# Performance work log

Hardware: AMD Instinct MI355X
Metric: run time of the kernel (lower is better)

The kernel has to match this reference:

```python
import jax, jax.numpy as jnp
import numpy as np

EPS = 1e-5
NUM_HEADS = 8
POOL_K = 50
POOL_S = 15
DEPTH = 4


def _conv2d(x, w, b, pad_h, pad_w):
    y = jax.lax.conv_general_dilated(
        x, w, window_strides=(1, 1),
        padding=((pad_h, pad_h), (pad_w, pad_w)),
        dimension_numbers=('NCHW', 'OIHW', 'NCHW'))
    return y + b[None, :, None, None]


def _bn_eval(x, g, b):
    # eval-mode BatchNorm2d with running_mean=0, running_var=1
    s = g / jnp.sqrt(1.0 + EPS)
    return x * s[None, :, None, None] + b[None, :, None, None]


def _layernorm(x, g, b):
    m = x.mean(-1, keepdims=True)
    v = ((x - m) ** 2).mean(-1, keepdims=True)
    return (x - m) / jnp.sqrt(v + EPS) * g + b


def _mha(x, wq, bq, wk, bk, wv, bv, wo, bo):
    B, n, d = x.shape
    def split(h):
        return h.reshape(B, n, NUM_HEADS, -1).transpose(0, 2, 1, 3)  # b h n dk
    q = split(x @ wq.T + bq)
    k = split(x @ wk.T + bk)
    v = split(x @ wv.T + bv)
    dk = q.shape[-1]
    scores = jnp.einsum('bhqd,bhkd->bhqk', q, k) / jnp.sqrt(jnp.float32(dk))
    attn = jax.nn.softmax(scores, axis=-1)
    o = jnp.einsum('bhqk,bhkd->bhqd', attn, v).transpose(0, 2, 1, 3).reshape(B, n, d)
    return o @ wo.T + bo


def _encoder(x, p):
    (g1, b1, g2, b2, wq, bq, wk, bk, wv, bv, wo, bo, f1w, f1b, f2w, f2b) = p
    h = _layernorm(x, g1, b1)
    x = x + _mha(h, wq, bq, wk, bk, wv, bv, wo, bo)
    h = _layernorm(x, g2, b2)
    ff = jax.nn.gelu(h @ f1w.T + f1b, approximate=False) @ f2w.T + f2b
    return x + ff


def _forward(x, tw1, tb1, tw2, tb2, tw3, tb3, tw4, tb4, bn1_g, bn1_b, sw, sb,
             bn2_g, bn2_b, ln1_g, ln1_b, ln2_g, ln2_b, wq, bq, wk, bk, wv, bv,
             wo, bo, f1w, f1b, f2w, f2b, ew, eb, bn3_g, bn3_b, cw, cb):
    B, C, T = x.shape
    xi = x[:, None]  # [B,1,C,T]
    h = jnp.concatenate([
        _conv2d(xi, tw1, tb1, 0, 7),
        _conv2d(xi, tw2, tb2, 0, 12),
        _conv2d(xi, tw3, tb3, 0, 25),
        _conv2d(xi, tw4, tb4, 0, 32)], axis=1)          # [B,D,C,T]
    h = _bn_eval(h, bn1_g, bn1_b)
    h = _conv2d(h, sw, sb, 0, 0)                         # [B,D,1,T]
    h = jax.nn.elu(_bn_eval(h, bn2_g, bn2_b))[:, :, 0]   # [B,D,T]

    npos = (T - POOL_K) // POOL_S + 1
    idx = np.arange(npos)[:, None] * POOL_S + np.arange(POOL_K)  # [n,K]
    win = h[:, :, idx]                                   # [B,D,n,K]
    avg = win.mean(-1)                                   # [B,D,n]
    var = win.var(-1, ddof=1)                            # unbiased, like torch
    vlog = jnp.log(jnp.clip(var, 1e-6, 1e6))
    x1 = avg.transpose(0, 2, 1)                          # [B,n,D]
    x2 = vlog.transpose(0, 2, 1)

    for i in range(DEPTH):
        p = (ln1_g[i], ln1_b[i], ln2_g[i], ln2_b[i], wq[i], bq[i], wk[i], bk[i],
             wv[i], bv[i], wo[i], bo[i], f1w[i], f1b[i], f2w[i], f2b[i])
        x1 = _encoder(x1, p)
        x2 = _encoder(x2, p)

    h = jnp.concatenate([x1[:, :, None, :], x2[:, :, None, :]], axis=2)  # [B,n,2,D]
    h = jax.nn.elu(_bn_eval(_conv2d(h, ew, eb, 0, 0), bn3_g, bn3_b))     # [B,n,1,D]
    return h.reshape(B, -1) @ cw.T + cb


def setup_inputs() -> dict:
    B, C, T, D, n, ff, ncls = 16, 64, 1000, 128, 64, 512, 4
    ks = iter(jax.random.split(jax.random.key(0), 48))
    def nrm(shape, s=0.02):
        return jax.random.normal(next(ks), shape, jnp.float32) * s
    inp = {
        'x': jax.random.normal(next(ks), (B, C, T), jnp.float32),
        'tw1': nrm((D // 4, 1, 1, 15)), 'tb1': jnp.zeros(D // 4),
        'tw2': nrm((D // 4, 1, 1, 25)), 'tb2': jnp.zeros(D // 4),
        'tw3': nrm((D // 4, 1, 1, 51)), 'tb3': jnp.zeros(D // 4),
        'tw4': nrm((D // 4, 1, 1, 65)), 'tb4': jnp.zeros(D // 4),
        'bn1_g': jnp.ones(D), 'bn1_b': jnp.zeros(D),
        'sw': nrm((D, D, C, 1)), 'sb': jnp.zeros(D),
        'bn2_g': jnp.ones(D), 'bn2_b': jnp.zeros(D),
        'ln1_g': jnp.ones((DEPTH, D)), 'ln1_b': jnp.zeros((DEPTH, D)),
        'ln2_g': jnp.ones((DEPTH, D)), 'ln2_b': jnp.zeros((DEPTH, D)),
        'wq': nrm((DEPTH, D, D)), 'bq': jnp.zeros((DEPTH, D)),
        'wk': nrm((DEPTH, D, D)), 'bk': jnp.zeros((DEPTH, D)),
        'wv': nrm((DEPTH, D, D)), 'bv': jnp.zeros((DEPTH, D)),
        'wo': nrm((DEPTH, D, D)), 'bo': jnp.zeros((DEPTH, D)),
        'f1w': nrm((DEPTH, ff, D)), 'f1b': jnp.zeros((DEPTH, ff)),
        'f2w': nrm((DEPTH, D, ff)), 'f2b': jnp.zeros((DEPTH, D)),
        'ew': nrm((n, n, 2, 1)), 'eb': jnp.zeros(n),
        'bn3_g': jnp.ones(n), 'bn3_b': jnp.zeros(n),
        'cw': nrm((ncls, D * n)), 'cb': jnp.zeros(ncls),
    }
    return inp


def reference(x, tw1, tb1, tw2, tb2, tw3, tb3, tw4, tb4, bn1_g, bn1_b, sw, sb,
              bn2_g, bn2_b, ln1_g, ln1_b, ln2_g, ln2_b, wq, bq, wk, bk, wv, bv,
              wo, bo, f1w, f1b, f2w, f2b, ew, eb, bn3_g, bn3_b, cw, cb):
    return _forward(x, tw1, tb1, tw2, tb2, tw3, tb3, tw4, tb4, bn1_g, bn1_b,
                    sw, sb, bn2_g, bn2_b, ln1_g, ln1_b, ln2_g, ln2_b, wq, bq,
                    wk, bk, wv, bv, wo, bo, f1w, f1b, f2w, f2b, ew, eb,
                    bn3_g, bn3_b, cw, cb)
```

## Files before the change

### kernel.cpp

```cpp
#include <hip/hip_runtime.h>
#include <math.h>

typedef unsigned short u16;
typedef __attribute__((ext_vector_type(8))) short frag8;
typedef __attribute__((ext_vector_type(4))) float f32x4;

__device__ __forceinline__ float eluf(float v) { return v > 0.f ? v : expm1f(v); }
__device__ __forceinline__ float geluf(float v) {
  return 0.5f * v * (1.f + erff(v * 0.70710678118654752f));
}
__device__ __forceinline__ u16 f2bf(float f) {
  union { float f; unsigned int i; } v; v.f = f;
  return (u16)((v.i + 0x7fffu + ((v.i >> 16) & 1u)) >> 16);
}

#define BN_S 0.99999500003749969f

__global__ void k_tws1(const float* tw1, const float* tw2, const float* tw3, const float* tw4,
                       const float* tb1, const float* tb2, const float* tb3, const float* tb4,
                       const float* bn1g, const float* bn1b,
                       float* tws1, float* c1) {
  int idx = blockIdx.x * 256 + threadIdx.x;
  if (idx < 8320) {
    int i = idx / 65, u = idx - i * 65;
    int g = i >> 5, il = i & 31;
    const float* tws[4] = {tw1, tw2, tw3, tw4};
    const int P[4] = {7, 12, 25, 32};
    int c = u - 32;
    float s1 = bn1g[i] * BN_S;
    float val = 0.f;
    int p = P[g];
    if (c >= -p && c <= p) val = s1 * tws[g][il * (2 * p + 1) + (c + p)];
    tws1[idx] = val;
  } else if (idx < 8448) {
    int i = idx - 8320;
    int g = i >> 5, il = i & 31;
    const float* tbs[4] = {tb1, tb2, tb3, tb4};
    float s1 = bn1g[i] * BN_S;
    c1[i] = s1 * tbs[g][il] + bn1b[i];
  }
}

__global__ __launch_bounds__(256) void k_weff(const float* __restrict__ sw, const float* __restrict__ sb,
                                              const float* __restrict__ tws1, const float* __restrict__ c1,
                                              u16* __restrict__ Wb, float* __restrict__ biasEff) {
  __shared__ float swl[8192];
  __shared__ float tl[8320];
  const int tid = threadIdx.x, lane = tid & 63, wave = tid >> 6;
  const int o = blockIdx.x;
  for (int idx = tid; idx < 8192; idx += 256) swl[idx] = sw[o * 8192 + idx];
  for (int idx = tid; idx < 8320; idx += 256) tl[idx] = tws1[idx];
  __syncthreads();

  #pragma unroll 1
  for (int j = 0; j < 4; j++) {
    int u0 = (wave + 4 * j) * 4;
    float a[4][4];
    #pragma unroll
    for (int uu = 0; uu < 4; uu++)
      #pragma unroll
      for (int r = 0; r < 4; r++) a[uu][r] = 0.f;
    #pragma unroll 1
    for (int i = 0; i < 128; i += 4) {
      #pragma unroll
      for (int ii = 0; ii < 4; ii++) {
        float s = swl[(i + ii) * 64 + lane];
        #pragma unroll
        for (int uu = 0; uu < 4; uu++)
          a[uu][ii] = fmaf(s, tl[(i + ii) * 65 + u0 + uu], a[uu][ii]);
      }
    }
    #pragma unroll
    for (int uu = 0; uu < 4; uu++)
      Wb[((u0 + uu) * 128 + o) * 64 + lane] = f2bf((a[uu][0] + a[uu][1]) + (a[uu][2] + a[uu][3]));
  }

  if (wave == 0) {
    float a[4] = {0.f, 0.f, 0.f, 0.f};
    #pragma unroll 1
    for (int i = 0; i < 128; i += 4) {
      #pragma unroll
      for (int ii = 0; ii < 4; ii++)
        a[ii] = fmaf(swl[(i + ii) * 64 + lane], tl[(i + ii) * 65 + 64], a[ii]);
    }
    Wb[(64 * 128 + o) * 64 + lane] = f2bf((a[0] + a[1]) + (a[2] + a[3]));
  } else if (wave == 1) {
    float pa = 0.f;
    #pragma unroll 8
    for (int i = 0; i < 128; i++)
      pa = fmaf(swl[i * 64 + lane], c1[i], pa);
    #pragma unroll
    for (int off = 32; off; off >>= 1) pa += __shfl_xor(pa, off);
    if (lane == 0) biasEff[o] = pa + sb[o];
  }
}

__global__ __launch_bounds__(256) void k_conv(const float* __restrict__ x,
                                              const u16* __restrict__ Wb,
                                              const float* __restrict__ biasEff,
                                              const float* __restrict__ bn2g, const float* __restrict__ bn2b,
                                              float* __restrict__ z) {
  __shared__ u16 xs[128 * 88];
  const int tid = threadIdx.x;
  const int t0 = blockIdx.x * 64;
  const int o0 = blockIdx.y * 32;
  const int b  = blockIdx.z;

  #pragma unroll
  for (int i = 0; i < 8; i++) {
    int pos = tid + i * 256;
    int kh = pos >> 5;
    int tt = (pos & 31) * 4;
    int gt = t0 - 32 + tt;
    const float* xp = x + (b * 64 + kh) * 1000;
    float v[4];
    if (gt >= 0 && gt + 3 < 1000) {
      float4 f = *(const float4*)(xp + gt);
      v[0] = f.x; v[1] = f.y; v[2] = f.z; v[3] = f.w;
    } else {
      #pragma unroll
      for (int e = 0; e < 4; e++) { int g2 = gt + e; v[e] = (g2 >= 0 && g2 < 1000) ? xp[g2] : 0.f; }
    }
    #pragma unroll
    for (int e = 0; e < 4; e++) xs[(tt + e) * 88 + kh] = f2bf(v[e]);
  }
  __syncthreads();

  const int lane = tid & 63, wave = tid >> 6;
  const int wt = (wave & 1) * 32;
  const int wo = (wave >> 1) * 16;
  const int m = lane & 15, q = lane >> 4;

  f32x4 acc[2];
  #pragma unroll
  for (int i = 0; i < 2; i++) acc[i] = (f32x4){0.f, 0.f, 0.f, 0.f};

  #pragma unroll 2
  for (int u = 0; u < 65; u++) {
    frag8 A[2][2], B[2];
    #pragma unroll
    for (int tp = 0; tp < 2; tp++)
      #pragma unroll
      for (int kc = 0; kc < 2; kc++)
        A[tp][kc] = *(const frag8*)&xs[(wt + tp * 16 + m + u) * 88 + kc * 32 + q * 8];
    #pragma unroll
    for (int kc = 0; kc < 2; kc++)
      B[kc] = *(const frag8*)(Wb + ((u * 128) + o0 + wo + m) * 64 + kc * 32 + q * 8);
    #pragma unroll
    for (int tp = 0; tp < 2; tp++) {
      acc[tp] = __builtin_amdgcn_mfma_f32_16x16x32_bf16(A[tp][0], B[0], acc[tp], 0, 0, 0);
      acc[tp] = __builtin_amdgcn_mfma_f32_16x16x32_bf16(A[tp][1], B[1], acc[tp], 0, 0, 0);
    }
  }

  {
    int o = o0 + wo + m;
    float s2 = bn2g[o] * BN_S;
    float be = biasEff[o], b2 = bn2b[o];
    #pragma unroll
    for (int tp = 0; tp < 2; tp++) {
      #pragma unroll
      for (int r = 0; r < 4; r++) {
        int t = t0 + wt + tp * 16 + q * 4 + r;
        if (t < 1000)
          z[(b * 128 + o) * 1000 + t] = eluf((acc[tp][r] + be) * s2 + b2);
      }
    }
  }
}

__global__ __launch_bounds__(256) void k_pool(const float* __restrict__ z, float* __restrict__ X) {
  __shared__ float zl[16 * 1001];
  int b = blockIdx.x, og = blockIdx.y;
  int tid = threadIdx.x;
  const float* zb = z + (b * 128 + og * 16) * 1000;
  #pragma unroll 1
  for (int r = 0; r < 16; r++)
    for (int c = tid; c < 1000; c += 256) zl[r * 1001 + c] = zb[r * 1000 + c];
  __syncthreads();

  int ol = tid & 15;
  int pb = tid >> 4;
  #pragma unroll 1
  for (int pass = 0; pass < 4; pass++) {
    int p = pb + pass * 16;
    const float* zp = zl + ol * 1001 + p * 15;
    float s = 0.f, ss = 0.f;
    #pragma unroll
    for (int k = 0; k < 50; k++) { float v = zp[k]; s += v; ss = fmaf(v, v, ss); }
    float m = s * 0.02f;
    float var = (ss - s * m) * (1.f / 49.f);
    var = fminf(fmaxf(var, 1e-6f), 1e6f);
    int o = og * 16 + ol;
    X[(b * 64 + p) * 128 + o] = m;
    X[((16 + b) * 64 + p) * 128 + o] = logf(var);
  }
}

__global__ __launch_bounds__(256) void k_cvt6(const float* __restrict__ wq, const float* __restrict__ wk,
                                              const float* __restrict__ wv, const float* __restrict__ wo,
                                              const float* __restrict__ f1w, const float* __restrict__ f2w,
                                              u16* __restrict__ out) {
  int i = blockIdx.x * 256 + threadIdx.x;
  if (i >= 196608) return;
  int fi = i * 4;
  const float* src; int off;
  if      (fi < 65536)  { src = wq;  off = fi; }
  else if (fi < 131072) { src = wk;  off = fi - 65536; }
  else if (fi < 196608) { src = wv;  off = fi - 131072; }
  else if (fi < 262144) { src = wo;  off = fi - 196608; }
  else if (fi < 524288) { src = f1w; off = fi - 262144; }
  else                  { src = f2w; off = fi - 524288; }
  float4 v = *(const float4*)(src + off);
  ushort4 p;
  p.x = f2bf(v.x); p.y = f2bf(v.y); p.z = f2bf(v.z); p.w = f2bf(v.w);
  *(ushort4*)(out + fi) = p;
}

__device__ __forceinline__ void ln128(const float* __restrict__ Xs, u16* __restrict__ Hs,
                                      const float* __restrict__ g, const float* __restrict__ b,
                                      int lane, int wave) {
  float g0 = g[lane], g1 = g[64 + lane], b0 = b[lane], b1 = b[64 + lane];
  #pragma unroll
  for (int rr = 0; rr < 8; rr++) {
    int r = wave * 8 + rr;
    float v0 = Xs[r * 132 + lane], v1 = Xs[r * 132 + 64 + lane];
    float s_ = v0 + v1;
    #pragma unroll
    for (int off = 32; off; off >>= 1) s_ += __shfl_xor(s_, off);
    float mn = s_ * (1.f / 128.f);
    float d0 = v0 - mn, d1 = v1 - mn;
    float qq = d0 * d0 + d1 * d1;
    #pragma unroll
    for (int off = 32; off; off >>= 1) qq += __shfl_xor(qq, off);
    float rs = rsqrtf(qq * (1.f / 128.f) + 1e-5f);
    Hs[r * 136 + lane]      = f2bf(d0 * rs * g0 + b0);
    Hs[r * 136 + 64 + lane] = f2bf(d1 * rs * g1 + b1);
  }
}

__device__ __forceinline__ void gemm_pref(const u16* __restrict__ Asrc, int astride,
                                          const frag8 Bf[4], int m, int q, f32x4 acc[4]) {
  #pragma unroll
  for (int kc = 0; kc < 4; kc++) {
    #pragma unroll
    for (int mt = 0; mt < 4; mt++) {
      frag8 Af = *(const frag8*)(Asrc + (mt * 16 + m) * astride + kc * 32 + q * 8);
      acc[mt] = __builtin_amdgcn_mfma_f32_16x16x32_bf16(Af, Bf[kc], acc[mt], 0, 0, 0);
    }
  }
}

__global__ __launch_bounds__(512, 1) void k_enc(float* __restrict__ X,
                                                const u16* __restrict__ Wenc,
                                                const float* __restrict__ ln1g, const float* __restrict__ ln1b,
                                                const float* __restrict__ ln2g, const float* __restrict__ ln2b,
                                                const float* __restrict__ bq, const float* __restrict__ bk,
                                                const float* __restrict__ bv, const float* __restrict__ bo,
                                                const float* __restrict__ f1b, const float* __restrict__ f2b) {
  __shared__ float Xs[64 * 132];
  __shared__ u16   Hs[64 * 136];
  __shared__ float QKV[3 * 64 * 132];
  float* Qs = QKV;
  float* Ks = QKV + 64 * 132;
  float* Vs = QKV + 2 * 64 * 132;
  u16* AOs  = Hs;
  u16* F1a  = (u16*)QKV;
  u16* F1b_ = (u16*)QKV + 64 * 136;

  const int tid = threadIdx.x;
  const int lane = tid & 63, wave = tid >> 6;
  const int m = lane & 15, q = lane >> 4;
  const int n0 = wave * 16;
  float* Xg = X + blockIdx.x * 64 * 128;

  const u16* WQ  = Wenc;
  const u16* WK  = Wenc + 65536;
  const u16* WV  = Wenc + 131072;
  const u16* WO  = Wenc + 196608;
  const u16* F1W = Wenc + 262144;
  const u16* F2W = Wenc + 524288;

  for (int i = tid; i < 8192; i += 512) Xs[(i >> 7) * 132 + (i & 127)] = Xg[i];
  __syncthreads();

  #pragma unroll 1
  for (int l = 0; l < 4; l++) {
    const u16* wqb  = WQ  + l * 16384;
    const u16* wkb  = WK  + l * 16384;
    const u16* wvb  = WV  + l * 16384;
    const u16* wob  = WO  + l * 16384;
    const u16* f1wb = F1W + l * 65536;
    const u16* f2wb = F2W + l * 65536;

    frag8 fq[4], fk[4], fv[4];
    #pragma unroll
    for (int kc = 0; kc < 4; kc++) {
      fq[kc] = *(const frag8*)(wqb + (n0 + m) * 128 + kc * 32 + q * 8);
      fk[kc] = *(const frag8*)(wkb + (n0 + m) * 128 + kc * 32 + q * 8);
      fv[kc] = *(const frag8*)(wvb + (n0 + m) * 128 + kc * 32 + q * 8);
    }

    ln128(Xs, Hs, ln1g + l * 128, ln1b + l * 128, lane, wave);
    __syncthreads();

    frag8 fo[4];
    #pragma unroll
    for (int kc = 0; kc < 4; kc++)
      fo[kc] = *(const frag8*)(wob + (n0 + m) * 128 + kc * 32 + q * 8);
    {
      f32x4 aq[4], ak[4], av[4];
      #pragma unroll
      for (int mt = 0; mt < 4; mt++) { aq[mt] = (f32x4){0,0,0,0}; ak[mt] = (f32x4){0,0,0,0}; av[mt] = (f32x4){0,0,0,0}; }
      gemm_pref(Hs, 136, fq, m, q, aq);
      gemm_pref(Hs, 136, fk, m, q, ak);
      gemm_pref(Hs, 136, fv, m, q, av);
      float bqv = bq[l * 128 + n0 + m];
      float bkv = bk[l * 128 + n0 + m];
      float bvv = bv[l * 128 + n0 + m];
      #pragma unroll
      for (int mt = 0; mt < 4; mt++)
        #pragma unroll
        for (int r = 0; r < 4; r++) {
          int row = mt * 16 + q * 4 + r;
          Qs[row * 132 + n0 + m] = aq[mt][r] + bqv;
          Ks[row * 132 + n0 + m] = ak[mt][r] + bkv;
          Vs[row * 132 + n0 + m] = av[mt][r] + bvv;
        }
    }
    __syncthreads();

    frag8 f1f[4];
    #pragma unroll
    for (int kc = 0; kc < 4; kc++)
      f1f[kc] = *(const frag8*)(f1wb + (n0 + m) * 128 + kc * 32 + q * 8);
    {
      const int h = wave, qr = lane;
      float qv[16];
      {
        const float4* qp = (const float4*)(Qs + qr * 132 + h * 16);
        #pragma unroll
        for (int j = 0; j < 4; j++) {
          float4 t = qp[j];
          qv[j * 4 + 0] = t.x; qv[j * 4 + 1] = t.y; qv[j * 4 + 2] = t.z; qv[j * 4 + 3] = t.w;
        }
      }
      const float* kbase = Ks + h * 16;
      const float* vbase = Vs + h * 16;
      float s_[64];
      float m0 = -1e30f, m1 = -1e30f, m2 = -1e30f, m3 = -1e30f;
      #pragma unroll
      for (int k4 = 0; k4 < 64; k4 += 4) {
        #pragma unroll
        for (int e = 0; e < 4; e++) {
          const float4* kp = (const float4*)(kbase + (k4 + e) * 132);
          float4 k0 = kp[0], k1 = kp[1], k2 = kp[2], k3 = kp[3];
          float d0 = qv[0] * k0.x + qv[1] * k0.y + qv[2] * k0.z + qv[3] * k0.w;
          float d1 = qv[4] * k1.x + qv[5] * k1.y + qv[6] * k1.z + qv[7] * k1.w;
          float d2 = qv[8] * k2.x + qv[9] * k2.y + qv[10] * k2.z + qv[11] * k2.w;
          float d3 = qv[12] * k3.x + qv[13] * k3.y + qv[14] * k3.z + qv[15] * k3.w;
          float sc = ((d0 + d1) + (d2 + d3)) * 0.25f;
          s_[k4 + e] = sc;
          if (e == 0) m0 = fmaxf(m0, sc);
          else if (e == 1) m1 = fmaxf(m1, sc);
          else if (e == 2) m2 = fmaxf(m2, sc);
          else m3 = fmaxf(m3, sc);
        }
      }
      float mx = fmaxf(fmaxf(m0, m1), fmaxf(m2, m3));
      float l_ = 0.f;
      float o[16];
      #pragma unroll
      for (int j = 0; j < 16; j++) o[j] = 0.f;
      #pragma unroll
      for (int k = 0; k < 64; k++) {
        float p = __expf(s_[k] - mx);
        l_ += p;
        const float4* vp = (const float4*)(vbase + k * 132);
        float4 v0 = vp[0], v1 = vp[1], v2 = vp[2], v3 = vp[3];
        o[0]  = fmaf(p, v0.x, o[0]);  o[1]  = fmaf(p, v0.y, o[1]);
        o[2]  = fmaf(p, v0.z, o[2]);  o[3]  = fmaf(p, v0.w, o[3]);
        o[4]  = fmaf(p, v1.x, o[4]);  o[5]  = fmaf(p, v1.y, o[5]);
        o[6]  = fmaf(p, v1.z, o[6]);  o[7]  = fmaf(p, v1.w, o[7]);
        o[8]  = fmaf(p, v2.x, o[8]);  o[9]  = fmaf(p, v2.y, o[9]);
        o[10] = fmaf(p, v2.z, o[10]); o[11] = fmaf(p, v2.w, o[11]);
        o[12] = fmaf(p, v3.x, o[12]); o[13] = fmaf(p, v3.y, o[13]);
        o[14] = fmaf(p, v3.z, o[14]); o[15] = fmaf(p, v3.w, o[15]);
      }
      float inv = 1.f / l_;
      u16* aop = AOs + qr * 136 + h * 16;
      #pragma unroll
      for (int j = 0; j < 16; j++) aop[j] = f2bf(o[j] * inv);
    }
    __syncthreads();

    {
      f32x4 ao4[4];
      #pragma unroll
      for (int mt = 0; mt < 4; mt++) ao4[mt] = (f32x4){0,0,0,0};
      gemm_pref(AOs, 136, fo, m, q, ao4);
      float bov = bo[l * 128 + n0 + m];
      #pragma unroll
      for (int mt = 0; mt < 4; mt++)
        #pragma unroll
        for (int r = 0; r < 4; r++)
          Xs[(mt * 16 + q * 4 + r) * 132 + n0 + m] += ao4[mt][r] + bov;
    }
    __syncthreads();

    ln128(Xs, Hs, ln2g + l * 128, ln2b + l * 128, lane, wave);
    __syncthreads();

    {
      f32x4 acc2[4];
      #pragma unroll
      for (int mt = 0; mt < 4; mt++) acc2[mt] = (f32x4){0,0,0,0};
      #pragma unroll 1
      for (int c = 0; c < 4; c++) {
        frag8 f2f[4];
        #pragma unroll
        for (int kc = 0; kc < 4; kc++)
          f2f[kc] = *(const frag8*)(f2wb + (n0 + m) * 512 + c * 128 + kc * 32 + q * 8);
        u16* F1c = (c & 1) ? F1b_ : F1a;
        {
          f32x4 a1[4];
          #pragma unroll
          for (int mt = 0; mt < 4; mt++) a1[mt] = (f32x4){0,0,0,0};
          gemm_pref(Hs, 136, f1f, m, q, a1);
          float b1v = f1b[l * 512 + c * 128 + n0 + m];
          #pragma unroll
          for (int mt = 0; mt < 4; mt++)
            #pragma unroll
            for (int r = 0; r < 4; r++)
              F1c[(mt * 16 + q * 4 + r) * 136 + n0 + m] = f2bf(geluf(a1[mt][r] + b1v));
        }
        __syncthreads();
        if (c < 3) {
          #pragma unroll
          for (int kc = 0; kc < 4; kc++)
            f1f[kc] = *(const frag8*)(f1wb + ((c + 1) * 128 + n0 + m) * 128 + kc * 32 + q * 8);
        }
        gemm_pref(F1c, 136, f2f, m, q, acc2);
      }
      float b2v = f2b[l * 128 + n0 + m];
      #pragma unroll
      for (int mt = 0; mt < 4; mt++)
        #pragma unroll
        for (int r = 0; r < 4; r++)
          Xs[(mt * 16 + q * 4 + r) * 132 + n0 + m] += acc2[mt][r] + b2v;
    }
    __syncthreads();
  }

  for (int i = tid; i < 8192; i += 512) Xg[i] = Xs[(i >> 7) * 132 + (i & 127)];
}

__global__ __launch_bounds__(256) void k_head1(const float* __restrict__ X, const float* __restrict__ ew,
                                               const float* __restrict__ eb, const float* __restrict__ g3,
                                               const float* __restrict__ b3, float* __restrict__ G) {
  __shared__ float Xs[2][8192];
  int b = blockIdx.x, ot = blockIdx.y;
  int tid = threadIdx.x;
  {
    const float4* x1 = (const float4*)(X + b * 8192);
    const float4* x2 = (const float4*)(X + (16 + b) * 8192);
    float4* s1 = (float4*)&Xs[0][0];
    float4* s2 = (float4*)&Xs[1][0];
    for (int i = tid; i < 2048; i += 256) { s1[i] = x1[i]; s2[i] = x2[i]; }
  }
  __syncthreads();
  int w = tid & 127, og = tid >> 7;
  int oc0 = ot * 16 + og * 8;
  float a[8] = {};
  for (int ic = 0; ic < 64; ic++) {
    float x1v = Xs[0][ic * 128 + w], x2v = Xs[1][ic * 128 + w];
    #pragma unroll
    for (int j = 0; j < 8; j++) {
      a[j] = fmaf(ew[((oc0 + j) * 64 + ic) * 2 + 0], x1v, a[j]);
      a[j] = fmaf(ew[((oc0 + j) * 64 + ic) * 2 + 1], x2v, a[j]);
    }
  }
  #pragma unroll
  for (int j = 0; j < 8; j++) {
    int oc = oc0 + j;
    float v = (a[j] + eb[oc]) * (g3[oc] * BN_S) + b3[oc];
    G[(b * 64 + oc) * 128 + w] = eluf(v);
  }
}

__global__ __launch_bounds__(256) void k_head2(const float* __restrict__ G, const float* __restrict__ cw,
                                               const float* __restrict__ cb, float* __restrict__ out) {
  __shared__ float red[256];
  int b = blockIdx.x, c = blockIdx.y, tid = threadIdx.x;
  const float4* g4 = (const float4*)(G + b * 8192);
  const float4* c4 = (const float4*)(cw + c * 8192);
  float p = 0.f;
  for (int i = tid; i < 2048; i += 256) {
    float4 g = g4[i], w = c4[i];
    p += g.x * w.x + g.y * w.y + g.z * w.z + g.w * w.w;
  }
  red[tid] = p;
  __syncthreads();
  for (int s = 128; s > 0; s >>= 1) {
    if (tid < s) red[tid] += red[tid + s];
    __syncthreads();
  }
  if (tid == 0) out[b * 4 + c] = red[0] + cb[c];
}

extern "C" void kernel_launch(void* const* d_in, const int* in_sizes, int n_in,
                              void* d_out, int out_size, void* d_ws, size_t ws_size,
                              hipStream_t stream) {
  const float* x    = (const float*)d_in[0];
  const float* tw1  = (const float*)d_in[1];  const float* tb1 = (const float*)d_in[2];
  const float* tw2  = (const float*)d_in[3];  const float* tb2 = (const float*)d_in[4];
  const float* tw3  = (const float*)d_in[5];  const float* tb3 = (const float*)d_in[6];
  const float* tw4  = (const float*)d_in[7];  const float* tb4 = (const float*)d_in[8];
  const float* bn1g = (const float*)d_in[9];  const float* bn1b = (const float*)d_in[10];
  const float* sw   = (const float*)d_in[11]; const float* sb   = (const float*)d_in[12];
  const float* bn2g = (const float*)d_in[13]; const float* bn2b = (const float*)d_in[14];
  const float* ln1g = (const float*)d_in[15]; const float* ln1b = (const float*)d_in[16];
  const float* ln2g = (const float*)d_in[17]; const float* ln2b = (const float*)d_in[18];
  const float* wq   = (const float*)d_in[19]; const float* bq   = (const float*)d_in[20];
  const float* wk   = (const float*)d_in[21]; const float* bk   = (const float*)d_in[22];
  const float* wv   = (const float*)d_in[23]; const float* bv   = (const float*)d_in[24];
  const float* wo   = (const float*)d_in[25]; const float* bo   = (const float*)d_in[26];
  const float* f1w  = (const float*)d_in[27]; const float* f1b  = (const float*)d_in[28];
  const float* f2w  = (const float*)d_in[29]; const float* f2b  = (const float*)d_in[30];
  const float* ew   = (const float*)d_in[31]; const float* eb   = (const float*)d_in[32];
  const float* g3   = (const float*)d_in[33]; const float* b3   = (const float*)d_in[34];
  const float* cw   = (const float*)d_in[35]; const float* cb   = (const float*)d_in[36];

  float* ws      = (float*)d_ws;
  float* tws1    = ws;
  float* c1      = ws + 8320;
  float* biasEff = ws + 8448;
  u16*   Wb      = (u16*)(ws + 8576);
  float* z       = ws + 541056;
  float* X       = ws + 2589056;
  u16*   Wenc    = (u16*)(ws + 3113344);
  float* G       = z;

  k_cvt6<<<768, 256, 0, stream>>>(wq, wk, wv, wo, f1w, f2w, Wenc);
  k_tws1<<<33, 256, 0, stream>>>(tw1, tw2, tw3, tw4, tb1, tb2, tb3, tb4, bn1g, bn1b, tws1, c1);
  k_weff<<<128, 256, 0, stream>>>(sw, sb, tws1, c1, Wb, biasEff);
  k_conv<<<dim3(16, 4, 16), 256, 0, stream>>>(x, Wb, biasEff, bn2g, bn2b, z);
  k_pool<<<dim3(16, 8), 256, 0, stream>>>(z, X);

  k_enc<<<32, 512, 0, stream>>>(X, Wenc, ln1g, ln1b, ln2g, ln2b, bq, bk, bv, bo, f1b, f2b);

  k_head1<<<dim3(16, 4), 256, 0, stream>>>(X, ew, eb, g3, b3, G);
  k_head2<<<dim3(16, 4), 256, 0, stream>>>(G, cw, cb, (float*)d_out);
}
```

Baseline: 404.8 us.

## Compute per-head attention with MFMA in bf16 and hoist LN A-fragments

Replaces the scalar fp32 per-thread attention (each thread looping over 64 keys with float4 LDS reads) with per-wave MFMA QK^T and PV in bf16. Q, K and a transposed V are written to per-wave bf16 LDS buffers, with padding to K=32, and the scale is folded into Q. Softmax is done on MFMA accumulators using 16-lane shuffles. Removing the per-head layout means the sync after QKV is dropped, and the LayerNorm A fragments are loaded once into registers and reused across the Q/K/V and FFN1 GEMMs. This cuts LDS traffic and scalar FMAs, at the cost of more register pressure and bf16 rounding of the scores and probabilities.

Result: faster. 384.2 us (-5.1%).

```diff
diff --git a/kernel.cpp b/kernel.cpp
--- a/kernel.cpp
+++ b/kernel.cpp
@@ -239,6 +239,14 @@
   }
 }
 
+__device__ __forceinline__ void gemm_hoist(const frag8 Ar[4][4], const frag8 Bf[4], f32x4 acc[4]) {
+  #pragma unroll
+  for (int kc = 0; kc < 4; kc++)
+    #pragma unroll
+    for (int mt = 0; mt < 4; mt++)
+      acc[mt] = __builtin_amdgcn_mfma_f32_16x16x32_bf16(Ar[mt][kc], Bf[kc], acc[mt], 0, 0, 0);
+}
+
 __device__ __forceinline__ void gemm_pref(const u16* __restrict__ Asrc, int astride,
                                           const frag8 Bf[4], int m, int q, f32x4 acc[4]) {
   #pragma unroll
@@ -258,15 +266,15 @@
                                                 const float* __restrict__ bq, const float* __restrict__ bk,
                                                 const float* __restrict__ bv, const float* __restrict__ bo,
                                                 const float* __restrict__ f1b, const float* __restrict__ f2b) {
-  __shared__ float Xs[64 * 132];
-  __shared__ u16   Hs[64 * 136];
-  __shared__ float QKV[3 * 64 * 132];
-  float* Qs = QKV;
-  float* Ks = QKV + 64 * 132;
-  float* Vs = QKV + 2 * 64 * 132;
-  u16* AOs  = Hs;
-  u16* F1a  = (u16*)QKV;
-  u16* F1b_ = (u16*)QKV + 64 * 136;
+  __shared__ __align__(16) float Xs[64 * 132];
+  __shared__ __align__(16) u16   Hs[64 * 136];
+  __shared__ __align__(16) u16   Qb[8 * 64 * 32];
+  __shared__ __align__(16) u16   Kb[8 * 64 * 32];
+  __shared__ __align__(16) u16   VtAO[8 * 16 * 80 + 64 * 136];
+  u16* Vt   = VtAO;
+  u16* AOs  = VtAO + 10240;
+  u16* F1a  = VtAO;
+  u16* F1b_ = VtAO + 8704;
 
   const int tid = threadIdx.x;
   const int lane = tid & 63, wave = tid >> 6;
@@ -280,6 +288,10 @@
   const u16* WO  = Wenc + 196608;
   const u16* F1W = Wenc + 262144;
   const u16* F2W = Wenc + 524288;
+
+  u16* Qh = Qb + wave * 2048;
+  u16* Kh = Kb + wave * 2048;
+  u16* Vh = Vt + wave * 1280;
 
   for (int i = tid; i < 8192; i += 512) Xs[(i >> 7) * 132 + (i & 127)] = Xg[i];
   __syncthreads();
@@ -309,12 +321,18 @@
     for (int kc = 0; kc < 4; kc++)
       fo[kc] = *(const frag8*)(wob + (n0 + m) * 128 + kc * 32 + q * 8);
     {
+      frag8 Ar[4][4];
+      #pragma unroll
+      for (int mt = 0; mt < 4; mt++)
+        #pragma unroll
+        for (int kc = 0; kc < 4; kc++)
+          Ar[mt][kc] = *(const frag8*)&Hs[(mt * 16 + m) * 136 + kc * 32 + q * 8];
       f32x4 aq[4], ak[4], av[4];
       #pragma unroll
       for (int mt = 0; mt < 4; mt++) { aq[mt] = (f32x4){0,0,0,0}; ak[mt] = (f32x4){0,0,0,0}; av[mt] = (f32x4){0,0,0,0}; }
-      gemm_pref(Hs, 136, fq, m, q, aq);
-      gemm_pref(Hs, 136, fk, m, q, ak);
-      gemm_pref(Hs, 136, fv, m, q, av);
+      gemm_hoist(Ar, fq, aq);
+      gemm_hoist(Ar, fk, ak);
+      gemm_hoist(Ar, fv, av);
       float bqv = bq[l * 128 + n0 + m];
       float bkv = bk[l * 128 + n0 + m];
       float bvv = bv[l * 128 + n0 + m];
@@ -323,74 +341,79 @@
         #pragma unroll
         for (int r = 0; r < 4; r++) {
           int row = mt * 16 + q * 4 + r;
-          Qs[row * 132 + n0 + m] = aq[mt][r] + bqv;
-          Ks[row * 132 + n0 + m] = ak[mt][r] + bkv;
-          Vs[row * 132 + n0 + m] = av[mt][r] + bvv;
+          Qh[row * 32 + m] = f2bf((aq[mt][r] + bqv) * 0.25f);
+          Kh[row * 32 + m] = f2bf(ak[mt][r] + bkv);
+          Vh[m * 80 + row] = f2bf(av[mt][r] + bvv);
         }
-    }
-    __syncthreads();
+      frag8 z8 = {};
+      *(frag8*)&Qh[lane * 32 + 16] = z8;
+      *(frag8*)&Qh[lane * 32 + 24] = z8;
+      *(frag8*)&Kh[lane * 32 + 16] = z8;
+      *(frag8*)&Kh[lane * 32 + 24] = z8;
+    }
 
     frag8 f1f[4];
     #pragma unroll
     for (int kc = 0; kc < 4; kc++)
       f1f[kc] = *(const frag8*)(f1wb + (n0 + m) * 128 + kc * 32 + q * 8);
     {
-      const int h = wave, qr = lane;
-      float qv[16];
-      {
-        const float4* qp = (const float4*)(Qs + qr * 132 + h * 16);
-        #pragma unroll
-        for (int j = 0; j < 4; j++) {
-          float4 t = qp[j];
-          qv[j * 4 + 0] = t.x; qv[j * 4 + 1] = t.y; qv[j * 4 + 2] = t.z; qv[j * 4 + 3] = t.w;
+      f32x4 sacc[4][4];
+      frag8 QA[4], KB[4];
+      #pragma unroll
+      for (int mt = 0; mt < 4; mt++) QA[mt] = *(const frag8*)&Qh[(mt * 16 + m) * 32 + q * 8];
+      #pragma unroll
+      for (int np = 0; np < 4; np++) KB[np] = *(const frag8*)&Kh[(np * 16 + m) * 32 + q * 8];
+      #pragma unroll
+      for (int mt = 0; mt < 4; mt++)
+        #pragma unroll
+        for (int np = 0; np < 4; np++)
+          sacc[mt][np] = __builtin_amdgcn_mfma_f32_16x16x32_bf16(QA[mt], KB[np], (f32x4){0,0,0,0}, 0, 0, 0);
+
+      float inv[4][4];
+      #pragma unroll
+      for (int mt = 0; mt < 4; mt++)
+        #pragma unroll
+        for (int r = 0; r < 4; r++) {
+          float mx = fmaxf(fmaxf(sacc[mt][0][r], sacc[mt][1][r]), fmaxf(sacc[mt][2][r], sacc[mt][3][r]));
+          #pragma unroll
+          for (int off = 1; off < 16; off <<= 1) mx = fmaxf(mx, __shfl_xor(mx, off));
+          #pragma unroll
+          for (int np = 0; np < 4; np++) sacc[mt][np][r] = __expf(sacc[mt][np][r] - mx);
+          float s_ = ((sacc[mt][0][r] + sacc[mt][1][r]) + (sacc[mt][2][r] + sacc[mt][3][r]));
+          #pragma unroll
+          for (int off = 1; off < 16; off <<= 1) s_ += __shfl_xor(s_, off);
+          inv[mt][r] = 1.f / s_;
+        }
+
+      #pragma unroll
+      for (int mt = 0; mt < 4; mt++)
+        #pragma unroll
+        for (int np = 0; np < 4; np++) {
+          u16* dst = (np < 2) ? Qh : Kh;
+          int col = (np & 1) * 16 + m;
+          #pragma unroll
+          for (int r = 0; r < 4; r++)
+            dst[(mt * 16 + q * 4 + r) * 32 + col] = f2bf(sacc[mt][np][r] * inv[mt][r]);
+        }
+
+      f32x4 oacc[4];
+      #pragma unroll
+      for (int mt = 0; mt < 4; mt++) oacc[mt] = (f32x4){0,0,0,0};
+      #pragma unroll
+      for (int kc = 0; kc < 2; kc++) {
+        frag8 VB = *(const frag8*)&Vh[m * 80 + kc * 32 + q * 8];
+        const u16* Psrc = kc ? Kh : Qh;
+        #pragma unroll
+        for (int mt = 0; mt < 4; mt++) {
+          frag8 PA = *(const frag8*)&Psrc[(mt * 16 + m) * 32 + q * 8];
+          oacc[mt] = __builtin_amdgcn_mfma_f32_16x16x32_bf16(PA, VB, oacc[mt], 0, 0, 0);
         }
       }
-      const float* kbase = Ks + h * 16;
-      const float* vbase = Vs + h * 16;
-      float s_[64];
-      float m0 = -1e30f, m1 = -1e30f, m2 = -1e30f, m3 = -1e30f;
-      #pragma unroll
-      for (int k4 = 0; k4 < 64; k4 += 4) {
-        #pragma unroll
-        for (int e = 0; e < 4; e++) {
-          const float4* kp = (const float4*)(kbase + (k4 + e) * 132);
-          float4 k0 = kp[0], k1 = kp[1], k2 = kp[2], k3 = kp[3];
-          float d0 = qv[0] * k0.x + qv[1] * k0.y + qv[2] * k0.z + qv[3] * k0.w;
-          float d1 = qv[4] * k1.x + qv[5] * k1.y + qv[6] * k1.z + qv[7] * k1.w;
-          float d2 = qv[8] * k2.x + qv[9] * k2.y + qv[10] * k2.z + qv[11] * k2.w;
-          float d3 = qv[12] * k3.x + qv[13] * k3.y + qv[14] * k3.z + qv[15] * k3.w;
-          float sc = ((d0 + d1) + (d2 + d3)) * 0.25f;
-          s_[k4 + e] = sc;
-          if (e == 0) m0 = fmaxf(m0, sc);
-          else if (e == 1) m1 = fmaxf(m1, sc);
-          else if (e == 2) m2 = fmaxf(m2, sc);
-          else m3 = fmaxf(m3, sc);
-        }
-      }
-      float mx = fmaxf(fmaxf(m0, m1), fmaxf(m2, m3));
-      float l_ = 0.f;
-      float o[16];
-      #pragma unroll
-      for (int j = 0; j < 16; j++) o[j] = 0.f;
-      #pragma unroll
-      for (int k = 0; k < 64; k++) {
-        float p = __expf(s_[k] - mx);
-        l_ += p;
-        const float4* vp = (const float4*)(vbase + k * 132);
-        float4 v0 = vp[0], v1 = vp[1], v2 = vp[2], v3 = vp[3];
-        o[0]  = fmaf(p, v0.x, o[0]);  o[1]  = fmaf(p, v0.y, o[1]);
-        o[2]  = fmaf(p, v0.z, o[2]);  o[3]  = fmaf(p, v0.w, o[3]);
-        o[4]  = fmaf(p, v1.x, o[4]);  o[5]  = fmaf(p, v1.y, o[5]);
-        o[6]  = fmaf(p, v1.z, o[6]);  o[7]  = fmaf(p, v1.w, o[7]);
-        o[8]  = fmaf(p, v2.x, o[8]);  o[9]  = fmaf(p, v2.y, o[9]);
-        o[10] = fmaf(p, v2.z, o[10]); o[11] = fmaf(p, v2.w, o[11]);
-        o[12] = fmaf(p, v3.x, o[12]); o[13] = fmaf(p, v3.y, o[13]);
-        o[14] = fmaf(p, v3.z, o[14]); o[15] = fmaf(p, v3.w, o[15]);
-      }
-      float inv = 1.f / l_;
-      u16* aop = AOs + qr * 136 + h * 16;
-      #pragma unroll
-      for (int j = 0; j < 16; j++) aop[j] = f2bf(o[j] * inv);
+      #pragma unroll
+      for (int mt = 0; mt < 4; mt++)
+        #pragma unroll
+        for (int r = 0; r < 4; r++)
+          AOs[(mt * 16 + q * 4 + r) * 136 + wave * 16 + m] = f2bf(oacc[mt][r]);
     }
     __syncthreads();
 
@@ -412,6 +435,12 @@
     __syncthreads();
 
     {
+      frag8 Ar[4][4];
+      #pragma unroll
+      for (int mt = 0; mt < 4; mt++)
+        #pragma unroll
+        for (int kc = 0; kc < 4; kc++)
+          Ar[mt][kc] = *(const frag8*)&Hs[(mt * 16 + m) * 136 + kc * 32 + q * 8];
       f32x4 acc2[4];
       #pragma unroll
       for (int mt = 0; mt < 4; mt++) acc2[mt] = (f32x4){0,0,0,0};
@@ -426,7 +455,7 @@
           f32x4 a1[4];
           #pragma unroll
           for (int mt = 0; mt < 4; mt++) a1[mt] = (f32x4){0,0,0,0};
-          gemm_pref(Hs, 136, f1f, m, q, a1);
+          gemm_hoist(Ar, f1f, a1);
           float b1v = f1b[l * 512 + c * 128 + n0 + m];
           #pragma unroll
           for (int mt = 0; mt < 4; mt++)
```
